# Optimization experiments

Hardware: AMD Instinct MI355X
Metric: run time of the kernel (lower is better)

Reference implementation:

```python
import jax, jax.numpy as jnp
import numpy as np

B = 65536
LATENT = 256
POSE_DIM, SHAPE_DIM, ROT_DIM, TRANS_DIM = 15, 10, 3, 3
N_JOINTS = 16  # MANO kinematic tree (wrist + 3 per finger x 5)
PARENTS = (-1, 0, 1, 2, 0, 4, 5, 0, 7, 8, 0, 10, 11, 0, 13, 14)


def setup_inputs() -> dict:
    key = jax.random.key(0)
    ks = jax.random.split(key, 13)
    f32 = jnp.float32
    inp = {
        'z_left': jax.random.normal(ks[0], (B, LATENT), dtype=f32),
        'z_right': jax.random.normal(ks[1], (B, LATENT), dtype=f32),
        # MLP params (Linear(256,512) -> ReLU -> Linear(512,256) -> ReLU -> Linear(256,31))
        'W1': jax.random.normal(ks[2], (LATENT, 512), dtype=f32) * 0.02,
        'b1': jnp.zeros((512,), dtype=f32),
        'W2': jax.random.normal(ks[3], (512, 256), dtype=f32) * 0.02,
        'b2': jnp.zeros((256,), dtype=f32),
        'W3': jax.random.normal(ks[4], (256, 31), dtype=f32) * 0.02,
        'b3': jnp.zeros((31,), dtype=f32),
        # MANO model parameters
        'J_template': jax.random.normal(ks[5], (N_JOINTS, 3), dtype=f32) * 0.05,
        'shape_dirs': jax.random.normal(ks[6], (N_JOINTS, 3, SHAPE_DIM), dtype=f32) * 0.01,
        'hands_components': jax.random.normal(ks[7], (POSE_DIM, 45), dtype=f32) * 0.1,  # PCA -> 15 joints axis-angle
        'hands_mean': jax.random.normal(ks[8], (45,), dtype=f32) * 0.1,
    }
    return inp


def rodrigues(r):
    """Axis-angle [..., 3] -> rotation matrices [..., 3, 3]."""
    theta = jnp.sqrt(jnp.sum(r * r, axis=-1, keepdims=True) + 1e-12)  # [...,1]
    k = r / theta
    kx, ky, kz = k[..., 0], k[..., 1], k[..., 2]
    z = jnp.zeros_like(kx)
    K = jnp.stack([z, -kz, ky, kz, z, -kx, -ky, kx, z], axis=-1)
    K = K.reshape(r.shape[:-1] + (3, 3))
    ct = jnp.cos(theta)[..., None]
    st = jnp.sin(theta)[..., None]
    I = jnp.eye(3, dtype=r.dtype)
    return I + st * K + (1.0 - ct) * (K @ K)


def _decode(z, W1, b1, W2, b2, W3, b3, J_template, shape_dirs, hands_components, hands_mean, is_right):
    # small MLP -> MANO params
    h = jax.nn.relu(z @ W1 + b1)
    h = jax.nn.relu(h @ W2 + b2)
    p = h @ W3 + b3                                    # [B,31]
    pose = p[:, :POSE_DIM]                             # [B,15] PCA coeffs
    shape = p[:, POSE_DIM:POSE_DIM + SHAPE_DIM]        # [B,10]
    rot = p[:, 25:28]                                  # global axis-angle
    trans = p[:, 28:31]

    # shape blend on joint template
    J = J_template[None] + jnp.einsum('jkd,bd->bjk', shape_dirs, shape)  # [B,16,3]
    if not is_right:
        J = J * jnp.asarray([-1.0, 1.0, 1.0], dtype=z.dtype)  # mirror for left hand

    # PCA pose -> per-joint axis-angle -> rotations
    full_pose = hands_mean[None] + pose @ hands_components   # [B,45]
    aa = full_pose.reshape(-1, 15, 3)
    R_global = rodrigues(rot)            # [B,3,3]
    R_local = rodrigues(aa)              # [B,15,3,3]
    R = jnp.concatenate([R_global[:, None], R_local], axis=1)  # [B,16,3,3]

    # batched kinematic chain (fixed 16-joint tree)
    Rw = [R[:, 0]]
    t = [J[:, 0]]
    for i in range(1, N_JOINTS):
        par = PARENTS[i]
        Rw.append(jnp.einsum('bij,bjk->bik', Rw[par], R[:, i]))
        t.append(jnp.einsum('bij,bj->bi', Rw[par], J[:, i] - J[:, par]) + t[par])
    joints = jnp.stack(t, axis=1) + trans[:, None, :]   # [B,16,3]
    return joints


def reference(z_left, z_right, W1, b1, W2, b2, W3, b3, J_template, shape_dirs, hands_components, hands_mean):
    joints_left = _decode(z_left, W1, b1, W2, b2, W3, b3, J_template, shape_dirs, hands_components, hands_mean, is_right=False)
    joints_right = _decode(z_right, W1, b1, W2, b2, W3, b3, J_template, shape_dirs, hands_components, hands_mean, is_right=True)
    return (joints_left, joints_right)
```

## Files before the change

### kernel.cpp

```cpp
#include <hip/hip_runtime.h>
#include <hip/hip_bf16.h>

typedef __attribute__((ext_vector_type(8))) short short8;
typedef __attribute__((ext_vector_type(4))) float f32x4;
typedef unsigned short ushort_t;

#define MFMA16(a,b,c) __builtin_amdgcn_mfma_f32_16x16x32_bf16((a),(b),(c),0,0,0)

__device__ __forceinline__ ushort_t f2bf(float x){
  unsigned int u = __builtin_bit_cast(unsigned int, x);
  unsigned int r = (u + 0x7FFFu + ((u >> 16) & 1u)) >> 16;
  return (ushort_t)r;
}
__device__ __forceinline__ float bf2f(ushort_t h){
  unsigned int u = ((unsigned int)h) << 16;
  return __builtin_bit_cast(float, u);
}

__device__ __forceinline__ void mat3mul(float* C, const float* A, const float* B){
  #pragma unroll
  for (int i = 0; i < 3; i++)
    #pragma unroll
    for (int k = 0; k < 3; k++)
      C[i*3+k] = A[i*3+0]*B[0*3+k] + A[i*3+1]*B[1*3+k] + A[i*3+2]*B[2*3+k];
}
__device__ __forceinline__ void rotp(float* o, const float* A, float x, float y, float z, const float* t){
  o[0] = A[0]*x + A[1]*y + A[2]*z + t[0];
  o[1] = A[3]*x + A[4]*y + A[5]*z + t[1];
  o[2] = A[6]*x + A[7]*y + A[8]*z + t[2];
}

__global__ __launch_bounds__(64) void poison_kernel(float* out, float val){
  if (threadIdx.x == 0 && blockIdx.x == 0) out[0] = val;
}

__global__ __launch_bounds__(256) void preconv_kernel(
    const float* __restrict__ W1, const float* __restrict__ W2, const float* __restrict__ W3,
    ushort_t* __restrict__ W1h, ushort_t* __restrict__ W1l,
    ushort_t* __restrict__ W2h, ushort_t* __restrict__ W2l,
    ushort_t* __restrict__ W3h, ushort_t* __restrict__ W3l)
{
  const int idx = blockIdx.x * 256 + threadIdx.x;
  {
    int j = idx & 7, l = (idx >> 3) & 63, kk = (idx >> 9) & 7, nt = idx >> 12;
    int k = kk*32 + (l >> 4)*8 + j, n = nt*16 + (l & 15);
    float w = W1[k*512 + n];
    ushort_t hi = f2bf(w);
    W1h[idx] = hi; W1l[idx] = f2bf(w - bf2f(hi));
  }
  {
    int j = idx & 7, l = (idx >> 3) & 63, kk = (idx >> 9) & 15, nt = idx >> 13;
    int k = kk*32 + (l >> 4)*8 + j, n = nt*16 + (l & 15);
    float w = W2[k*256 + n];
    ushort_t hi = f2bf(w);
    W2h[idx] = hi; W2l[idx] = f2bf(w - bf2f(hi));
  }
  if (idx < 16384){
    int j = idx & 7, l = (idx >> 3) & 63, kk = (idx >> 9) & 7, nt = idx >> 12;
    int k = kk*32 + (l >> 4)*8 + j, n = nt*16 + (l & 15);
    float w = (nt < 2 && n < 31) ? W3[k*31 + n] : 0.f;
    ushort_t hi = f2bf(w);
    W3h[idx] = hi; W3l[idx] = f2bf(w - bf2f(hi));
  }
}

__global__ __launch_bounds__(256, 2) void fused_kernel(
    const float* __restrict__ zL, const float* __restrict__ zR,
    const ushort_t* __restrict__ W1h, const ushort_t* __restrict__ W1l,
    const ushort_t* __restrict__ W2h, const ushort_t* __restrict__ W2l,
    const ushort_t* __restrict__ W3h, const ushort_t* __restrict__ W3l,
    const float* __restrict__ b1, const float* __restrict__ b2, const float* __restrict__ b3,
    const float* __restrict__ Jt, const float* __restrict__ sd,
    const float* __restrict__ hc, const float* __restrict__ hm,
    float* __restrict__ out)
{
  __shared__ ushort_t regA[2*32*264];
  __shared__ ushort_t regB[2*32*72];
  __shared__ float    Rlds[32*145];
  __shared__ float    plbuf[32*33];
  ushort_t* regAhi = regA;
  ushort_t* regAlo = regA + 32*264;
  ushort_t* regBhi = regB;
  ushort_t* regBlo = regB + 32*72;

  const int tid  = threadIdx.x;
  const int lane = tid & 63;
  const int w    = tid >> 6;
  const int lo   = lane & 15;
  const int g    = lane >> 4;
  const int m0   = blockIdx.x * 32;
  const bool right = (m0 >= 65536);
  const float* zsrc = right ? (zR + (size_t)(m0 - 65536) * 256)
                            : (zL + (size_t)m0 * 256);

  #pragma unroll
  for (int i = 0; i < 8; i++){
    int e = i*1024 + tid*4;
    float4 v = *(const float4*)(zsrc + e);
    int r = e >> 8, c = e & 255;
    ushort_t* dh = &regAhi[r*264 + c];
    ushort_t* dl = &regAlo[r*264 + c];
    float vv[4] = {v.x, v.y, v.z, v.w};
    #pragma unroll
    for (int q = 0; q < 4; q++){
      ushort_t hi = f2bf(vv[q]);
      dh[q] = hi; dl[q] = f2bf(vv[q] - bf2f(hi));
    }
  }
  __syncthreads();

  f32x4 accL2[2][4];
  #pragma unroll
  for (int a = 0; a < 2; a++)
    #pragma unroll
    for (int b = 0; b < 4; b++)
      accL2[a][b] = (f32x4){0.f,0.f,0.f,0.f};

  for (int c = 0; c < 8; c++){
    {
      const int nt = c*4 + w;
      short8 bh[8], bl[8];
      #pragma unroll
      for (int kk = 0; kk < 8; kk++){
        bh[kk] = *(const short8*)(W1h + (size_t)(nt*8 + kk)*512 + lane*8);
        bl[kk] = *(const short8*)(W1l + (size_t)(nt*8 + kk)*512 + lane*8);
      }
      const float bias = b1[nt*16 + lo];
      #pragma unroll
      for (int rt = 0; rt < 2; rt++){
        f32x4 acc = (f32x4){0.f,0.f,0.f,0.f};
        #pragma unroll
        for (int kk = 0; kk < 8; kk++){
          short8 ah = *(const short8*)&regAhi[(rt*16 + lo)*264 + kk*32 + g*8];
          short8 al = *(const short8*)&regAlo[(rt*16 + lo)*264 + kk*32 + g*8];
          acc = MFMA16(ah, bh[kk], acc);
          acc = MFMA16(ah, bl[kk], acc);
          acc = MFMA16(al, bh[kk], acc);
        }
        #pragma unroll
        for (int i = 0; i < 4; i++){
          float v = fmaxf(acc[i] + bias, 0.f);
          ushort_t hi = f2bf(v);
          const int ro = (rt*16 + g*4 + i)*72 + w*16 + lo;
          regBhi[ro] = hi; regBlo[ro] = f2bf(v - bf2f(hi));
        }
      }
    }
    __syncthreads();
    {
      #pragma unroll
      for (int x = 0; x < 2; x++){
        short8 b2h[4], b2l[4];
        #pragma unroll
        for (int q = 0; q < 4; q++){
          b2h[q] = *(const short8*)(W2h + (size_t)((w*4+q)*16 + c*2 + x)*512 + lane*8);
          b2l[q] = *(const short8*)(W2l + (size_t)((w*4+q)*16 + c*2 + x)*512 + lane*8);
        }
        #pragma unroll
        for (int rt = 0; rt < 2; rt++){
          short8 ah = *(const short8*)&regBhi[(rt*16 + lo)*72 + x*32 + g*8];
          short8 al = *(const short8*)&regBlo[(rt*16 + lo)*72 + x*32 + g*8];
          #pragma unroll
          for (int q = 0; q < 4; q++){
            accL2[rt][q] = MFMA16(ah, b2h[q], accL2[rt][q]);
            accL2[rt][q] = MFMA16(ah, b2l[q], accL2[rt][q]);
            accL2[rt][q] = MFMA16(al, b2h[q], accL2[rt][q]);
          }
        }
      }
    }
    __syncthreads();
  }

  #pragma unroll
  for (int rt = 0; rt < 2; rt++){
    #pragma unroll
    for (int q = 0; q < 4; q++){
      const int col = w*64 + q*16 + lo;
      const float bias = b2[col];
      #pragma unroll
      for (int i = 0; i < 4; i++){
        float v = fmaxf(accL2[rt][q][i] + bias, 0.f);
        ushort_t hi = f2bf(v);
        const int ro = (rt*16 + g*4 + i)*264 + col;
        regAhi[ro] = hi; regAlo[ro] = f2bf(v - bf2f(hi));
      }
    }
  }
  __syncthreads();

  {
    const int rw = w & 1, nn = w >> 1;
    f32x4 acc3 = (f32x4){0.f,0.f,0.f,0.f};
    #pragma unroll
    for (int kk = 0; kk < 8; kk++){
      short8 ah = *(const short8*)&regAhi[(rw*16 + lo)*264 + kk*32 + g*8];
      short8 al = *(const short8*)&regAlo[(rw*16 + lo)*264 + kk*32 + g*8];
      short8 bh = *(const short8*)(W3h + (size_t)(nn*8 + kk)*512 + lane*8);
      short8 bl = *(const short8*)(W3l + (size_t)(nn*8 + kk)*512 + lane*8);
      acc3 = MFMA16(ah, bh, acc3);
      acc3 = MFMA16(ah, bl, acc3);
      acc3 = MFMA16(al, bh, acc3);
    }
    const int col = nn*16 + lo;
    const float bias = (col < 31) ? b3[col] : 0.f;
    #pragma unroll
    for (int i = 0; i < 4; i++)
      plbuf[(rw*16 + g*4 + i)*33 + col] = acc3[i] + bias;
  }
  __syncthreads();
  const float* pl = plbuf;

  for (int u = tid; u < 512; u += 256){
    const int r = u >> 4, j = u & 15;
    float ax, ay, az;
    if (j == 0){
      ax = pl[r*33+25]; ay = pl[r*33+26]; az = pl[r*33+27];
    } else {
      const int base = 3*(j-1);
      float s0 = hm[base+0], s1 = hm[base+1], s2 = hm[base+2];
      #pragma unroll
      for (int d = 0; d < 15; d++){
        float pv = pl[r*33 + d];
        s0 = fmaf(pv, hc[d*45 + base+0], s0);
        s1 = fmaf(pv, hc[d*45 + base+1], s1);
        s2 = fmaf(pv, hc[d*45 + base+2], s2);
      }
      ax = s0; ay = s1; az = s2;
    }
    float th = sqrtf(ax*ax + ay*ay + az*az + 1e-12f);
    float inv = 1.0f / th;
    float kx = ax*inv, ky = ay*inv, kz = az*inv;
    float st = __sinf(th), ct = __cosf(th);
    float omc = 1.0f - ct;
    float* Rr = &Rlds[r*145 + j*9];
    Rr[0] = ct + omc*kx*kx;      Rr[1] = omc*kx*ky - st*kz;  Rr[2] = omc*kx*kz + st*ky;
    Rr[3] = omc*kx*ky + st*kz;   Rr[4] = ct + omc*ky*ky;     Rr[5] = omc*ky*kz - st*kx;
    Rr[6] = omc*kx*kz - st*ky;   Rr[7] = omc*ky*kz + st*kx;  Rr[8] = ct + omc*kz*kz;
  }
  __syncthreads();

  if (tid < 32){
    const int r = tid;
    float sh[10];
    #pragma unroll
    for (int d = 0; d < 10; d++) sh[d] = pl[r*33 + 15 + d];
    const float trx = pl[r*33+28], tr_y = pl[r*33+29], trz = pl[r*33+30];
    float J[16][3];
    #pragma unroll
    for (int jj = 0; jj < 16; jj++){
      #pragma unroll
      for (int k2 = 0; k2 < 3; k2++){
        float v = Jt[jj*3 + k2];
        #pragma unroll
        for (int d = 0; d < 10; d++) v = fmaf(sd[(jj*3 + k2)*10 + d], sh[d], v);
        J[jj][k2] = v;
      }
    }
    if (!right){
      #pragma unroll
      for (int jj = 0; jj < 16; jj++) J[jj][0] = -J[jj][0];
    }
    const float* Rbase = &Rlds[r*145];
    float R0[9];
    #pragma unroll
    for (int e = 0; e < 9; e++) R0[e] = Rbase[e];
    const size_t ob = (right ? (size_t)3145728 : (size_t)0)
                    + (size_t)(m0 - (right ? 65536 : 0) + r) * 48;
    float t0[3] = {J[0][0], J[0][1], J[0][2]};
    out[ob+0] = t0[0]+trx; out[ob+1] = t0[1]+tr_y; out[ob+2] = t0[2]+trz;
    #pragma unroll
    for (int f = 0; f < 5; f++){
      const int i1 = 3*f+1, i2 = 3*f+2, i3 = 3*f+3;
      float R1[9], R2[9], Rw1[9], Rw2[9], t1[3], t2[3], t3[3];
      #pragma unroll
      for (int e = 0; e < 9; e++) R1[e] = Rbase[i1*9 + e];
      #pragma unroll
      for (int e = 0; e < 9; e++) R2[e] = Rbase[i2*9 + e];
      mat3mul(Rw1, R0, R1);
      rotp(t1, R0,  J[i1][0]-J[0][0],  J[i1][1]-J[0][1],  J[i1][2]-J[0][2],  t0);
      mat3mul(Rw2, Rw1, R2);
      rotp(t2, Rw1, J[i2][0]-J[i1][0], J[i2][1]-J[i1][1], J[i2][2]-J[i1][2], t1);
      rotp(t3, Rw2, J[i3][0]-J[i2][0], J[i3][1]-J[i2][1], J[i3][2]-J[i2][2], t2);
      out[ob + i1*3+0] = t1[0]+trx; out[ob + i1*3+1] = t1[1]+tr_y; out[ob + i1*3+2] = t1[2]+trz;
      out[ob + i2*3+0] = t2[0]+trx; out[ob + i2*3+1] = t2[1]+tr_y; out[ob + i2*3+2] = t2[2]+trz;
      out[ob + i3*3+0] = t3[0]+trx; out[ob + i3*3+1] = t3[1]+tr_y; out[ob + i3*3+2] = t3[2]+trz;
    }
  }
}

extern "C" void kernel_launch(void* const* d_in, const int* in_sizes, int n_in,
                              void* d_out, int out_size, void* d_ws, size_t ws_size,
                              hipStream_t stream) {
  const float* zL = (const float*)d_in[0];
  const float* zR = (const float*)d_in[1];
  const float* W1 = (const float*)d_in[2];
  const float* b1 = (const float*)d_in[3];
  const float* W2 = (const float*)d_in[4];
  const float* b2 = (const float*)d_in[5];
  const float* W3 = (const float*)d_in[6];
  const float* b3 = (const float*)d_in[7];
  const float* Jt = (const float*)d_in[8];
  const float* sd = (const float*)d_in[9];
  const float* hc = (const float*)d_in[10];
  const float* hm = (const float*)d_in[11];

  float* out = (float*)d_out;

  if (ws_size < 1114112){
    poison_kernel<<<1, 64, 0, stream>>>(out, 20480.f);
    return;
  }

  ushort_t* W1h = (ushort_t*)d_ws;
  ushort_t* W1l = W1h + 131072;
  ushort_t* W2h = W1l + 131072;
  ushort_t* W2l = W2h + 131072;
  ushort_t* W3h = W2l + 131072;
  ushort_t* W3l = W3h + 16384;

  preconv_kernel<<<512, 256, 0, stream>>>(W1, W2, W3, W1h, W1l, W2h, W2l, W3h, W3l);
  fused_kernel<<<4096, 256, 0, stream>>>(zL, zR, W1h, W1l, W2h, W2l, W3h, W3l,
                                         b1, b2, b3, Jt, sd, hc, hm, out);
}
```

Before: 301.1 us.

## Drop Rodrigues LDS stage, compute rotations per-row in-thread, raise occupancy to 3

Removes the Rlds shared buffer and the 256-thread Rodrigues pass plus its barrier. Each of the first 32 threads now computes only the rotations its kinematic chain needs, directly in registers. It also splits the three split-bf16 MFMA chains into independent accumulators to shorten dependency chains, and raises launch_bounds min blocks to 3 to allow more resident blocks. The cost is more serial work for 32 threads and possible register pressure or spills under the tighter occupancy bound.

After: 269.5 us. -10.5%, faster.

```diff
diff --git a/kernel.cpp b/kernel.cpp
--- a/kernel.cpp
+++ b/kernel.cpp
@@ -64,7 +64,7 @@
   }
 }
 
-__global__ __launch_bounds__(256, 2) void fused_kernel(
+__global__ __launch_bounds__(256, 3) void fused_kernel(
     const float* __restrict__ zL, const float* __restrict__ zR,
     const ushort_t* __restrict__ W1h, const ushort_t* __restrict__ W1l,
     const ushort_t* __restrict__ W2h, const ushort_t* __restrict__ W2l,
@@ -76,7 +76,6 @@
 {
   __shared__ ushort_t regA[2*32*264];
   __shared__ ushort_t regB[2*32*72];
-  __shared__ float    Rlds[32*145];
   __shared__ float    plbuf[32*33];
   ushort_t* regAhi = regA;
   ushort_t* regAlo = regA + 32*264;
@@ -128,18 +127,20 @@
       const float bias = b1[nt*16 + lo];
       #pragma unroll
       for (int rt = 0; rt < 2; rt++){
-        f32x4 acc = (f32x4){0.f,0.f,0.f,0.f};
+        f32x4 ahh = (f32x4){0.f,0.f,0.f,0.f};
+        f32x4 ahl = (f32x4){0.f,0.f,0.f,0.f};
+        f32x4 alh = (f32x4){0.f,0.f,0.f,0.f};
         #pragma unroll
         for (int kk = 0; kk < 8; kk++){
           short8 ah = *(const short8*)&regAhi[(rt*16 + lo)*264 + kk*32 + g*8];
           short8 al = *(const short8*)&regAlo[(rt*16 + lo)*264 + kk*32 + g*8];
-          acc = MFMA16(ah, bh[kk], acc);
-          acc = MFMA16(ah, bl[kk], acc);
-          acc = MFMA16(al, bh[kk], acc);
+          ahh = MFMA16(ah, bh[kk], ahh);
+          ahl = MFMA16(ah, bl[kk], ahl);
+          alh = MFMA16(al, bh[kk], alh);
         }
         #pragma unroll
         for (int i = 0; i < 4; i++){
-          float v = fmaxf(acc[i] + bias, 0.f);
+          float v = fmaxf(ahh[i] + ahl[i] + alh[i] + bias, 0.f);
           ushort_t hi = f2bf(v);
           const int ro = (rt*16 + g*4 + i)*72 + w*16 + lo;
           regBhi[ro] = hi; regBlo[ro] = f2bf(v - bf2f(hi));
@@ -191,80 +192,80 @@
 
   {
     const int rw = w & 1, nn = w >> 1;
-    f32x4 acc3 = (f32x4){0.f,0.f,0.f,0.f};
+    f32x4 ahh = (f32x4){0.f,0.f,0.f,0.f};
+    f32x4 ahl = (f32x4){0.f,0.f,0.f,0.f};
+    f32x4 alh = (f32x4){0.f,0.f,0.f,0.f};
     #pragma unroll
     for (int kk = 0; kk < 8; kk++){
       short8 ah = *(const short8*)&regAhi[(rw*16 + lo)*264 + kk*32 + g*8];
       short8 al = *(const short8*)&regAlo[(rw*16 + lo)*264 + kk*32 + g*8];
       short8 bh = *(const short8*)(W3h + (size_t)(nn*8 + kk)*512 + lane*8);
       short8 bl = *(const short8*)(W3l + (size_t)(nn*8 + kk)*512 + lane*8);
-      acc3 = MFMA16(ah, bh, acc3);
-      acc3 = MFMA16(ah, bl, acc3);
-      acc3 = MFMA16(al, bh, acc3);
+      ahh = MFMA16(ah, bh, ahh);
+      ahl = MFMA16(ah, bl, ahl);
+      alh = MFMA16(al, bh, alh);
     }
     const int col = nn*16 + lo;
     const float bias = (col < 31) ? b3[col] : 0.f;
     #pragma unroll
     for (int i = 0; i < 4; i++)
-      plbuf[(rw*16 + g*4 + i)*33 + col] = acc3[i] + bias;
+      plbuf[(rw*16 + g*4 + i)*33 + col] = ahh[i] + ahl[i] + alh[i] + bias;
   }
   __syncthreads();
   const float* pl = plbuf;
 
-  for (int u = tid; u < 512; u += 256){
-    const int r = u >> 4, j = u & 15;
-    float ax, ay, az;
-    if (j == 0){
-      ax = pl[r*33+25]; ay = pl[r*33+26]; az = pl[r*33+27];
-    } else {
+  if (tid < 32){
+    const int r = tid;
+    float p15[15];
+    #pragma unroll
+    for (int d = 0; d < 15; d++) p15[d] = pl[r*33 + d];
+    float sh[10];
+    #pragma unroll
+    for (int d = 0; d < 10; d++) sh[d] = pl[r*33 + 15 + d];
+    const float trx = pl[r*33+28], tr_y = pl[r*33+29], trz = pl[r*33+30];
+
+    float J[16][3];
+    #pragma unroll
+    for (int jj = 0; jj < 16; jj++){
+      #pragma unroll
+      for (int k2 = 0; k2 < 3; k2++){
+        float v = Jt[jj*3 + k2];
+        #pragma unroll
+        for (int d = 0; d < 10; d++) v = fmaf(sd[(jj*3 + k2)*10 + d], sh[d], v);
+        J[jj][k2] = v;
+      }
+    }
+    if (!right){
+      #pragma unroll
+      for (int jj = 0; jj < 16; jj++) J[jj][0] = -J[jj][0];
+    }
+
+    auto rod = [](float ax, float ay, float az, float* R){
+      float th = sqrtf(ax*ax + ay*ay + az*az + 1e-12f);
+      float inv = 1.0f / th;
+      float kx = ax*inv, ky = ay*inv, kz = az*inv;
+      float st = __sinf(th), ct = __cosf(th);
+      float omc = 1.0f - ct;
+      R[0] = ct + omc*kx*kx;      R[1] = omc*kx*ky - st*kz;  R[2] = omc*kx*kz + st*ky;
+      R[3] = omc*kx*ky + st*kz;   R[4] = ct + omc*ky*ky;     R[5] = omc*ky*kz - st*kx;
+      R[6] = omc*kx*kz - st*ky;   R[7] = omc*ky*kz + st*kx;  R[8] = ct + omc*kz*kz;
+    };
+    auto axis_rod = [&](int j, float* R){
       const int base = 3*(j-1);
       float s0 = hm[base+0], s1 = hm[base+1], s2 = hm[base+2];
       #pragma unroll
       for (int d = 0; d < 15; d++){
-        float pv = pl[r*33 + d];
+        float pv = p15[d];
         s0 = fmaf(pv, hc[d*45 + base+0], s0);
         s1 = fmaf(pv, hc[d*45 + base+1], s1);
         s2 = fmaf(pv, hc[d*45 + base+2], s2);
       }
-      ax = s0; ay = s1; az = s2;
-    }
-    float th = sqrtf(ax*ax + ay*ay + az*az + 1e-12f);
-    float inv = 1.0f / th;
-    float kx = ax*inv, ky = ay*inv, kz = az*inv;
-    float st = __sinf(th), ct = __cosf(th);
-    float omc = 1.0f - ct;
-    float* Rr = &Rlds[r*145 + j*9];
-    Rr[0] = ct + omc*kx*kx;      Rr[1] = omc*kx*ky - st*kz;  Rr[2] = omc*kx*kz + st*ky;
-    Rr[3] = omc*kx*ky + st*kz;   Rr[4] = ct + omc*ky*ky;     Rr[5] = omc*ky*kz - st*kx;
-    Rr[6] = omc*kx*kz - st*ky;   Rr[7] = omc*ky*kz + st*kx;  Rr[8] = ct + omc*kz*kz;
-  }
-  __syncthreads();
-
-  if (tid < 32){
-    const int r = tid;
-    float sh[10];
-    #pragma unroll
-    for (int d = 0; d < 10; d++) sh[d] = pl[r*33 + 15 + d];
-    const float trx = pl[r*33+28], tr_y = pl[r*33+29], trz = pl[r*33+30];
-    float J[16][3];
-    #pragma unroll
-    for (int jj = 0; jj < 16; jj++){
-      #pragma unroll
-      for (int k2 = 0; k2 < 3; k2++){
-        float v = Jt[jj*3 + k2];
-        #pragma unroll
-        for (int d = 0; d < 10; d++) v = fmaf(sd[(jj*3 + k2)*10 + d], sh[d], v);
-        J[jj][k2] = v;
-      }
-    }
-    if (!right){
-      #pragma unroll
-      for (int jj = 0; jj < 16; jj++) J[jj][0] = -J[jj][0];
-    }
-    const float* Rbase = &Rlds[r*145];
+      rod(s0, s1, s2, R);
+    };
+
     float R0[9];
-    #pragma unroll
-    for (int e = 0; e < 9; e++) R0[e] = Rbase[e];
+    rod(pl[r*33+25], pl[r*33+26], pl[r*33+27], R0);
+
     const size_t ob = (right ? (size_t)3145728 : (size_t)0)
                     + (size_t)(m0 - (right ? 65536 : 0) + r) * 48;
     float t0[3] = {J[0][0], J[0][1], J[0][2]};
@@ -273,10 +274,8 @@
     for (int f = 0; f < 5; f++){
       const int i1 = 3*f+1, i2 = 3*f+2, i3 = 3*f+3;
       float R1[9], R2[9], Rw1[9], Rw2[9], t1[3], t2[3], t3[3];
-      #pragma unroll
-      for (int e = 0; e < 9; e++) R1[e] = Rbase[i1*9 + e];
-      #pragma unroll
-      for (int e = 0; e < 9; e++) R2[e] = Rbase[i2*9 + e];
+      axis_rod(i1, R1);
+      axis_rod(i2, R2);
       mat3mul(Rw1, R0, R1);
       rotp(t1, R0,  J[i1][0]-J[0][0],  J[i1][1]-J[0][1],  J[i1][2]-J[0][2],  t0);
       mat3mul(Rw2, Rw1, R2);
```
